# Kernel tuning notes

Hardware: AMD Instinct MI355X
Metric: run time of the kernel (lower is better)

Reference implementation:

```python
import jax, jax.numpy as jnp
import numpy as np

D_MODEL = 2048
NUM_HEADS = 16
D_K = D_MODEL // NUM_HEADS  # 128
BATCH, SEQ = 2, 2048


def setup_inputs() -> dict:
    key = jax.random.key(0)
    ks = jax.random.split(key, 9)
    s = 0.02
    return {
        "x": jax.random.normal(ks[0], (BATCH, SEQ, D_MODEL), dtype=jnp.float32),
        "W_q": jax.random.normal(ks[1], (D_MODEL, D_MODEL), dtype=jnp.float32) * s,
        "b_q": jax.random.normal(ks[2], (D_MODEL,), dtype=jnp.float32) * s,
        "W_k": jax.random.normal(ks[3], (D_MODEL, D_K), dtype=jnp.float32) * s,
        "b_k": jax.random.normal(ks[4], (D_K,), dtype=jnp.float32) * s,
        "W_v": jax.random.normal(ks[5], (D_MODEL, D_K), dtype=jnp.float32) * s,
        "b_v": jax.random.normal(ks[6], (D_K,), dtype=jnp.float32) * s,
        "W_o": jax.random.normal(ks[7], (D_MODEL, D_MODEL), dtype=jnp.float32) * s,
        "b_o": jax.random.normal(ks[8], (D_MODEL,), dtype=jnp.float32) * s,
    }


def reference(x, W_q, b_q, W_k, b_k, W_v, b_v, W_o, b_o):
    B, S, _ = x.shape
    # Q: per-head projections -> (B, H, S, d_k)
    Q = (x @ W_q + b_q).reshape(B, S, NUM_HEADS, D_K).transpose(0, 2, 1, 3)
    # K, V: single shared head -> (B, S, d_k)
    K = x @ W_k + b_k
    V = x @ W_v + b_v
    scale = 1.0 / np.sqrt(D_K)
    # scores: (B, H, S_q, S_k); K broadcast across heads (no expand materialized)
    scores = jnp.einsum("bhqd,bkd->bhqk", Q, K) * scale
    attn = jax.nn.softmax(scores, axis=-1)
    out = jnp.einsum("bhqk,bkd->bhqd", attn, V)  # (B, H, S, d_k)
    out = out.transpose(0, 2, 1, 3).reshape(B, S, D_MODEL)
    out = out @ W_o + b_o
    K_cache = K[:, None, :, :]  # (B, 1, S, d_k)
    V_cache = V[:, None, :, :]
    return (out, K_cache, V_cache)
```

## Files before the change

### kernel.cpp

```cpp
#include <hip/hip_runtime.h>
#include <cstdint>

typedef __bf16 bf16x8 __attribute__((ext_vector_type(8)));
typedef float f32x4 __attribute__((ext_vector_type(4)));
typedef unsigned short ushort_t;

constexpr int kS  = 2048;
constexpr int kDM = 2048;
constexpr int kDK = 128;
constexpr int kNH = 16;
constexpr int kB  = 2;
constexpr int kNQKV = kDM + 2 * kDK;

__device__ __forceinline__ unsigned short f2bf(float f) {
  union { float f; unsigned u; } v; v.f = f;
  unsigned u = v.u;
  u += 0x7fffu + ((u >> 16) & 1u);
  return (unsigned short)(u >> 16);
}

__device__ __forceinline__ void gload16(const void* g, void* l) {
  __builtin_amdgcn_global_load_lds(
      (const __attribute__((address_space(1))) void*)g,
      (__attribute__((address_space(3))) void*)l, 16, 0, 0);
}

__global__ __launch_bounds__(256) void cast_f32_bf16(const float* __restrict__ in,
                                                     ushort_t* __restrict__ out, long n) {
  long i = ((long)blockIdx.x * 256 + threadIdx.x) * 4;
  if (i >= n) return;
  float4 f = *reinterpret_cast<const float4*>(in + i);
  ushort4 o;
  o.x = f2bf(f.x); o.y = f2bf(f.y); o.z = f2bf(f.z); o.w = f2bf(f.w);
  *reinterpret_cast<ushort4*>(out + i) = o;
}

__global__ __launch_bounds__(256) void transpose_cast(const float* __restrict__ in,
                                                      ushort_t* __restrict__ out,
                                                      int R, int C) {
  __shared__ float tile[32][33];
  int c = blockIdx.x * 32 + threadIdx.x;
  int r0 = blockIdx.y * 32;
  #pragma unroll
  for (int i = threadIdx.y; i < 32; i += 8)
    tile[i][threadIdx.x] = in[(long)(r0 + i) * C + c];
  __syncthreads();
  int oc  = r0 + threadIdx.x;
  int or0 = blockIdx.x * 32;
  #pragma unroll
  for (int i = threadIdx.y; i < 32; i += 8)
    out[(long)(or0 + i) * R + oc] = f2bf(tile[threadIdx.x][i]);
}

__device__ __forceinline__ void gemm128(const ushort_t* __restrict__ A, int lda,
                                        const ushort_t* __restrict__ Bt, int ldb,
                                        int K, int row0, int col0,
                                        f32x4 (&acc)[4][4]) {
  __shared__ __align__(16) ushort_t sA[128 * 32];
  __shared__ __align__(16) ushort_t sB[128 * 32];
  int t = threadIdx.x;
  int r = t >> 2, c4 = t & 3;
  const ushort_t* gA0 = A  + (long)(row0 + r)      * lda + c4 * 8;
  const ushort_t* gA1 = A  + (long)(row0 + r + 64) * lda + c4 * 8;
  const ushort_t* gB0 = Bt + (long)(col0 + r)      * ldb + c4 * 8;
  const ushort_t* gB1 = Bt + (long)(col0 + r + 64) * ldb + c4 * 8;
  int lane = t & 63, wave = t >> 6;
  int wr = wave >> 1, wc = wave & 1;
  int lr = lane & 15, lg = lane >> 4;
  int aoff = (wr * 64 + lr) * 32 + lg * 8;
  int boff = (wc * 64 + lr) * 32 + lg * 8;

  for (int kk = 0; kk < K; kk += 32) {
    gload16(gA0 + kk, (void*)(sA + t * 8));
    gload16(gA1 + kk, (void*)(sA + 2048 + t * 8));
    gload16(gB0 + kk, (void*)(sB + t * 8));
    gload16(gB1 + kk, (void*)(sB + 2048 + t * 8));
    __syncthreads();
    bf16x8 af[4], bg[4];
    #pragma unroll
    for (int i = 0; i < 4; i++) af[i] = *(const bf16x8*)(sA + aoff + i * 16 * 32);
    #pragma unroll
    for (int j = 0; j < 4; j++) bg[j] = *(const bf16x8*)(sB + boff + j * 16 * 32);
    #pragma unroll
    for (int i = 0; i < 4; i++)
      #pragma unroll
      for (int j = 0; j < 4; j++)
        acc[i][j] = __builtin_amdgcn_mfma_f32_16x16x32_bf16(af[i], bg[j], acc[i][j], 0, 0, 0);
    __syncthreads();
  }
}

__global__ __launch_bounds__(256) void gemm_qkv(const ushort_t* __restrict__ x,
    const ushort_t* __restrict__ Wt, const float* __restrict__ bq,
    const float* __restrict__ bk, const float* __restrict__ bv,
    ushort_t* __restrict__ Qb, float* __restrict__ Kc,
    ushort_t* __restrict__ Kb, float* __restrict__ Vc, ushort_t* __restrict__ Vtb) {
  f32x4 acc[4][4] = {};
  int row0 = blockIdx.y * 128, col0 = blockIdx.x * 128;
  gemm128(x, kDM, Wt, kDM, kDM, row0, col0, acc);
  int lane = threadIdx.x & 63, wave = threadIdx.x >> 6;
  int wr = wave >> 1, wc = wave & 1, lr = lane & 15, lg = lane >> 4;
  #pragma unroll
  for (int i = 0; i < 4; i++) {
    #pragma unroll
    for (int j = 0; j < 4; j++) {
      int col = col0 + wc * 64 + j * 16 + lr;
      float bias = (col < kDM) ? bq[col]
                 : (col < kDM + kDK) ? bk[col - kDM] : bv[col - kDM - kDK];
      #pragma unroll
      for (int rr = 0; rr < 4; rr++) {
        int row = row0 + wr * 64 + i * 16 + lg * 4 + rr;
        float v = acc[i][j][rr] + bias;
        if (col < kDM) {
          Qb[(long)row * kDM + col] = f2bf(v);
        } else if (col < kDM + kDK) {
          int c = col - kDM;
          Kc[(long)row * kDK + c] = v;
          Kb[(long)row * kDK + c] = f2bf(v);
        } else {
          int c = col - kDM - kDK;
          Vc[(long)row * kDK + c] = v;
          Vtb[((long)(row >> 11) * kDK + c) * kS + (row & 2047)] = f2bf(v);
        }
      }
    }
  }
}

__global__ __launch_bounds__(256) void gemm_out(const ushort_t* __restrict__ A,
    const ushort_t* __restrict__ Wt, const float* __restrict__ bias,
    float* __restrict__ C) {
  f32x4 acc[4][4] = {};
  int row0 = blockIdx.y * 128, col0 = blockIdx.x * 128;
  gemm128(A, kDM, Wt, kDM, kDM, row0, col0, acc);
  int lane = threadIdx.x & 63, wave = threadIdx.x >> 6;
  int wr = wave >> 1, wc = wave & 1, lr = lane & 15, lg = lane >> 4;
  #pragma unroll
  for (int i = 0; i < 4; i++) {
    #pragma unroll
    for (int j = 0; j < 4; j++) {
      int col = col0 + wc * 64 + j * 16 + lr;
      float bv = bias[col];
      #pragma unroll
      for (int rr = 0; rr < 4; rr++) {
        int row = row0 + wr * 64 + i * 16 + lg * 4 + rr;
        C[(long)row * kDM + col] = acc[i][j][rr] + bv;
      }
    }
  }
}

__global__ __launch_bounds__(256, 2) void flash_attn(
    const ushort_t* __restrict__ Qb, const ushort_t* __restrict__ Kb,
    const ushort_t* __restrict__ Vt, ushort_t* __restrict__ Ob) {
  __shared__ __align__(16) ushort_t sK[128 * 128];
  __shared__ __align__(16) ushort_t sV[128 * 128];

  const int tid = threadIdx.x;
  const int L = tid & 63, wave = tid >> 6;
  const int lr = L & 15, lg = L >> 4;
  const int bh = blockIdx.y, b = bh >> 4, h = bh & 15;
  const int q0 = blockIdx.x * 128;

  const ushort_t* Kg = Kb + (long)b * kS * kDK;
  const ushort_t* Vg = Vt + (long)b * kDK * kS;
  const ushort_t* Qg = Qb + ((long)b * kS + q0 + wave * 32) * kDM + h * kDK;

  bf16x8 qf[2][4];
  #pragma unroll
  for (int i = 0; i < 2; i++)
    #pragma unroll
    for (int kk = 0; kk < 4; kk++)
      qf[i][kk] = *(const bf16x8*)(Qg + (long)(i * 16 + lr) * kDM + kk * 32 + lg * 8);

  f32x4 accO[8][2] = {};
  float lsum[2] = {};

  constexpr float kScaleLog2e = 0.12751743f;

  for (int j = 0; j < 16; j++) {
    __syncthreads();
    #pragma unroll
    for (int s8 = 0; s8 < 8; s8++) {
      int c = tid + s8 * 256;
      int f = c >> 6, cl = c & 63;
      int st = f >> 2, kk = f & 3, n = cl & 15;
      int key = (st >> 1) * 32 + (n >> 2) * 8 + (st & 1) * 4 + (n & 3);
      gload16(Kg + (long)(j * 128 + key) * kDK + kk * 32 + (cl >> 4) * 8,
              (void*)(sK + c * 8));
      int d = c >> 4, kb = (c & 15) ^ (d & 15);
      gload16(Vg + (long)d * kS + j * 128 + kb * 8, (void*)(sV + c * 8));
    }
    __syncthreads();

    #pragma unroll
    for (int u = 0; u < 4; u++) {
      f32x4 sacc[2][2] = {};
      __builtin_amdgcn_s_setprio(1);
      #pragma unroll
      for (int kk = 0; kk < 4; kk++)
        #pragma unroll
        for (int jj = 0; jj < 2; jj++) {
          bf16x8 kf = *(const bf16x8*)(sK + ((u * 2 + jj) * 4 + kk) * 512 + L * 8);
          #pragma unroll
          for (int i = 0; i < 2; i++)
            sacc[jj][i] = __builtin_amdgcn_mfma_f32_16x16x32_bf16(kf, qf[i][kk], sacc[jj][i], 0, 0, 0);
        }
      __builtin_amdgcn_s_setprio(0);

      bf16x8 pf[2];
      #pragma unroll
      for (int i = 0; i < 2; i++) {
        union { bf16x8 v; unsigned w[4]; } P;
        #pragma unroll
        for (int jj = 0; jj < 2; jj++) {
          float p0 = __builtin_amdgcn_exp2f(sacc[jj][i][0] * kScaleLog2e);
          float p1 = __builtin_amdgcn_exp2f(sacc[jj][i][1] * kScaleLog2e);
          float p2 = __builtin_amdgcn_exp2f(sacc[jj][i][2] * kScaleLog2e);
          float p3 = __builtin_amdgcn_exp2f(sacc[jj][i][3] * kScaleLog2e);
          lsum[i] += (p0 + p1) + (p2 + p3);
          asm("v_cvt_pk_bf16_f32 %0, %1, %2" : "=v"(P.w[jj * 2 + 0]) : "v"(p0), "v"(p1));
          asm("v_cvt_pk_bf16_f32 %0, %1, %2" : "=v"(P.w[jj * 2 + 1]) : "v"(p2), "v"(p3));
        }
        pf[i] = P.v;
      }

      __builtin_amdgcn_s_setprio(1);
      #pragma unroll
      for (int t = 0; t < 8; t++) {
        int kbL = (u * 4 + lg) ^ lr;
        bf16x8 vf = *(const bf16x8*)(sV + t * 2048 + lr * 128 + kbL * 8);
        #pragma unroll
        for (int i = 0; i < 2; i++)
          accO[t][i] = __builtin_amdgcn_mfma_f32_16x16x32_bf16(vf, pf[i], accO[t][i], 0, 0, 0);
      }
      __builtin_amdgcn_s_setprio(0);
    }
  }

  float inv[2];
  #pragma unroll
  for (int i = 0; i < 2; i++) {
    float v = lsum[i];
    v += __shfl_xor(v, 16);
    v += __shfl_xor(v, 32);
    inv[i] = 1.0f / v;
  }

  ushort_t* Og = Ob + ((long)b * kS + q0 + wave * 32) * kDM + h * kDK;
  #pragma unroll
  for (int t = 0; t < 8; t++)
    #pragma unroll
    for (int i = 0; i < 2; i++) {
      union { ushort4 o; unsigned w[2]; } O;
      float f0 = accO[t][i][0] * inv[i];
      float f1 = accO[t][i][1] * inv[i];
      float f2 = accO[t][i][2] * inv[i];
      float f3 = accO[t][i][3] * inv[i];
      asm("v_cvt_pk_bf16_f32 %0, %1, %2" : "=v"(O.w[0]) : "v"(f0), "v"(f1));
      asm("v_cvt_pk_bf16_f32 %0, %1, %2" : "=v"(O.w[1]) : "v"(f2), "v"(f3));
      *(ushort4*)(Og + (long)(i * 16 + lr) * kDM + t * 16 + lg * 4) = O.o;
    }
}

extern "C" void kernel_launch(void* const* d_in, const int* in_sizes, int n_in,
                              void* d_out, int out_size, void* d_ws, size_t ws_size,
                              hipStream_t stream) {
  (void)in_sizes; (void)n_in; (void)out_size; (void)ws_size;
  const float* x   = (const float*)d_in[0];
  const float* W_q = (const float*)d_in[1];
  const float* b_q = (const float*)d_in[2];
  const float* W_k = (const float*)d_in[3];
  const float* b_k = (const float*)d_in[4];
  const float* W_v = (const float*)d_in[5];
  const float* b_v = (const float*)d_in[6];
  const float* W_o = (const float*)d_in[7];
  const float* b_o = (const float*)d_in[8];

  float* out = (float*)d_out;
  float* Kc  = out + (long)kB * kS * kDM;
  float* Vc  = Kc  + (long)kB * kS * kDK;

  char* w = (char*)d_ws;
  ushort_t* x_bf   = (ushort_t*)w;  w += 16777216;
  ushort_t* Wall_t = (ushort_t*)w;  w += (size_t)kNQKV*kDM*2;
  ushort_t* Wo_t   = (ushort_t*)w;  w += 8388608;
  ushort_t* Q_bf   = (ushort_t*)w;  w += 16777216;
  ushort_t* K_bf   = (ushort_t*)w;  w += 1048576;
  ushort_t* Vt_bf  = (ushort_t*)w;  w += 1048576;
  ushort_t* O_bf   = (ushort_t*)w;  w += 16777216;

  dim3 blk(256);
  dim3 tblk(32, 8);

  cast_f32_bf16<<<dim3(8192), blk, 0, stream>>>(x, x_bf, (long)kB * kS * kDM);
  transpose_cast<<<dim3(64, 64), tblk, 0, stream>>>(W_q, Wall_t, kDM, kDM);
  transpose_cast<<<dim3(4, 64),  tblk, 0, stream>>>(W_k, Wall_t + (long)kDM * kDM, kDM, kDK);
  transpose_cast<<<dim3(4, 64),  tblk, 0, stream>>>(W_v, Wall_t + (long)(kDM + kDK) * kDM, kDM, kDK);
  transpose_cast<<<dim3(64, 64), tblk, 0, stream>>>(W_o, Wo_t, kDM, kDM);

  gemm_qkv<<<dim3(kNQKV / 128, kB * kS / 128), blk, 0, stream>>>(
      x_bf, Wall_t, b_q, b_k, b_v, Q_bf, Kc, K_bf, Vc, Vt_bf);

  flash_attn<<<dim3(kS / 128, kB * kNH), blk, 0, stream>>>(Q_bf, K_bf, Vt_bf, O_bf);

  gemm_out<<<dim3(kDM / 128, kB * kS / 128), blk, 0, stream>>>(O_bf, Wo_t, b_o, out);
}
```

Measured before the change: 317.2 us.

## Double-buffer K/V tiles in flash attention to overlap loads with MFMA compute

```diff
diff --git a/kernel.cpp b/kernel.cpp
--- a/kernel.cpp
+++ b/kernel.cpp
@@ -153,8 +153,8 @@
 __global__ __launch_bounds__(256, 2) void flash_attn(
     const ushort_t* __restrict__ Qb, const ushort_t* __restrict__ Kb,
     const ushort_t* __restrict__ Vt, ushort_t* __restrict__ Ob) {
-  __shared__ __align__(16) ushort_t sK[128 * 128];
-  __shared__ __align__(16) ushort_t sV[128 * 128];
+  __shared__ __align__(16) ushort_t sK[2][64 * 128];
+  __shared__ __align__(16) ushort_t sV[2][64 * 128];
 
   const int tid = threadIdx.x;
   const int L = tid & 63, wave = tid >> 6;
@@ -173,35 +173,44 @@
     for (int kk = 0; kk < 4; kk++)
       qf[i][kk] = *(const bf16x8*)(Qg + (long)(i * 16 + lr) * kDM + kk * 32 + lg * 8);
 
+  int koff[4], voff[4];
+  #pragma unroll
+  for (int s = 0; s < 4; s++) {
+    int c = tid + s * 256;
+    int f = c >> 6, cl = c & 63;
+    int st = f >> 2, kk = f & 3, n = cl & 15;
+    int key = (st >> 1) * 32 + (n >> 2) * 8 + (st & 1) * 4 + (n & 3);
+    koff[s] = key * kDK + kk * 32 + (cl >> 4) * 8;
+    int d = c >> 3, kb = (c & 7) ^ (d & 7);
+    voff[s] = d * kS + kb * 8;
+  }
+
   f32x4 accO[8][2] = {};
   float lsum[2] = {};
 
   constexpr float kScaleLog2e = 0.12751743f;
 
-  for (int j = 0; j < 16; j++) {
-    __syncthreads();
-    #pragma unroll
-    for (int s8 = 0; s8 < 8; s8++) {
-      int c = tid + s8 * 256;
-      int f = c >> 6, cl = c & 63;
-      int st = f >> 2, kk = f & 3, n = cl & 15;
-      int key = (st >> 1) * 32 + (n >> 2) * 8 + (st & 1) * 4 + (n & 3);
-      gload16(Kg + (long)(j * 128 + key) * kDK + kk * 32 + (cl >> 4) * 8,
-              (void*)(sK + c * 8));
-      int d = c >> 4, kb = (c & 15) ^ (d & 15);
-      gload16(Vg + (long)d * kS + j * 128 + kb * 8, (void*)(sV + c * 8));
-    }
-    __syncthreads();
-
-    #pragma unroll
-    for (int u = 0; u < 4; u++) {
+  auto stage = [&](int jt, int bb) {
+    const ushort_t* Kt = Kg + (long)jt * 64 * kDK;
+    const ushort_t* Vtg = Vg + jt * 64;
+    #pragma unroll
+    for (int s = 0; s < 4; s++) {
+      int c8 = (tid + s * 256) * 8;
+      gload16(Kt + koff[s], (void*)(sK[bb] + c8));
+      gload16(Vtg + voff[s], (void*)(sV[bb] + c8));
+    }
+  };
+
+  auto compute = [&](int bb) {
+    #pragma unroll
+    for (int u = 0; u < 2; u++) {
       f32x4 sacc[2][2] = {};
       __builtin_amdgcn_s_setprio(1);
       #pragma unroll
       for (int kk = 0; kk < 4; kk++)
         #pragma unroll
         for (int jj = 0; jj < 2; jj++) {
-          bf16x8 kf = *(const bf16x8*)(sK + ((u * 2 + jj) * 4 + kk) * 512 + L * 8);
+          bf16x8 kf = *(const bf16x8*)(sK[bb] + ((u * 2 + jj) * 4 + kk) * 512 + L * 8);
           #pragma unroll
           for (int i = 0; i < 2; i++)
             sacc[jj][i] = __builtin_amdgcn_mfma_f32_16x16x32_bf16(kf, qf[i][kk], sacc[jj][i], 0, 0, 0);
@@ -228,14 +237,25 @@
       __builtin_amdgcn_s_setprio(1);
       #pragma unroll
       for (int t = 0; t < 8; t++) {
-        int kbL = (u * 4 + lg) ^ lr;
-        bf16x8 vf = *(const bf16x8*)(sV + t * 2048 + lr * 128 + kbL * 8);
+        int kbL = (u * 4 + lg) ^ (lr & 7);
+        bf16x8 vf = *(const bf16x8*)(sV[bb] + t * 1024 + lr * 64 + kbL * 8);
         #pragma unroll
         for (int i = 0; i < 2; i++)
           accO[t][i] = __builtin_amdgcn_mfma_f32_16x16x32_bf16(vf, pf[i], accO[t][i], 0, 0, 0);
       }
       __builtin_amdgcn_s_setprio(0);
     }
+  };
+
+  stage(0, 0);
+  __syncthreads();
+  for (int jt = 0; jt < 32; jt += 2) {
+    stage(jt + 1, 1);
+    compute(0);
+    __syncthreads();
+    if (jt + 2 < 32) stage(jt + 2, 0);
+    compute(1);
+    __syncthreads();
   }
 
   float inv[2];
```

After: 313.6 us. Within noise of the previous version (-1.1%).
